# Kernel optimization log

Hardware: AMD Instinct MI355X
Metric: run time of the kernel (lower is better)

Reference implementation:

```python
import jax, jax.numpy as jnp
import numpy as np

PH, PW = 7, 7            # pooled_height, pooled_width
SCALE = 0.0625           # spatial_scale = 1/16


def setup_inputs() -> dict:
    key = jax.random.key(0)
    k1, k2, k3, k4 = jax.random.split(key, 4)
    N, C, H, W, R = 4, 512, 64, 64, 2000
    features = jax.random.normal(k1, (N, C, H, W), jnp.float32)
    # rois: (batch_idx, x1, y1, x2, y2) in image coords (image = H/SCALE x W/SCALE)
    b = jax.random.randint(k2, (R,), 0, N).astype(jnp.float32)
    xs = jnp.sort(jax.random.uniform(k3, (R, 2), jnp.float32, 0.0, W / SCALE - 1.0), axis=1)
    ys = jnp.sort(jax.random.uniform(k4, (R, 2), jnp.float32, 0.0, H / SCALE - 1.0), axis=1)
    rois = jnp.stack([b, xs[:, 0], ys[:, 0], xs[:, 1], ys[:, 1]], axis=1)
    return {"features": features, "rois": rois}


def _roi_pool(features, rois):
    # split ROI into PH x PW bins with floor/ceil boundaries, max-pool each bin.
    N, C, H, W = features.shape
    # Max spatial extent of one bin: ceil(H/PH)+1 rows; +2 is a safe static bound.
    Kh = int(np.ceil(H / PH)) + 2
    Kw = int(np.ceil(W / PW)) + 2

    def per_roi(roi):
        b = roi[0].astype(jnp.int32)
        x1 = jnp.round(roi[1] * SCALE).astype(jnp.int32)
        y1 = jnp.round(roi[2] * SCALE).astype(jnp.int32)
        x2 = jnp.round(roi[3] * SCALE).astype(jnp.int32)
        y2 = jnp.round(roi[4] * SCALE).astype(jnp.int32)
        roi_w = jnp.maximum(x2 - x1 + 1, 1).astype(jnp.float32)
        roi_h = jnp.maximum(y2 - y1 + 1, 1).astype(jnp.float32)
        bin_h = roi_h / PH
        bin_w = roi_w / PW
        ih = jnp.arange(PH, dtype=jnp.float32)
        iw = jnp.arange(PW, dtype=jnp.float32)
        hstart = jnp.clip(jnp.floor(ih * bin_h).astype(jnp.int32) + y1, 0, H)        # [PH]
        hend = jnp.clip(jnp.ceil((ih + 1.0) * bin_h).astype(jnp.int32) + y1, 0, H)   # [PH]
        wstart = jnp.clip(jnp.floor(iw * bin_w).astype(jnp.int32) + x1, 0, W)        # [PW]
        wend = jnp.clip(jnp.ceil((iw + 1.0) * bin_w).astype(jnp.int32) + x1, 0, W)   # [PW]
        # Fixed-size windows per bin, with validity masks
        hidx = hstart[:, None] + jnp.arange(Kh)[None, :]          # [PH, Kh]
        hval = hidx < hend[:, None]
        hidx = jnp.clip(hidx, 0, H - 1)
        widx = wstart[:, None] + jnp.arange(Kw)[None, :]          # [PW, Kw]
        wval = widx < wend[:, None]
        widx = jnp.clip(widx, 0, W - 1)
        fmap = features[b]                                        # [C, H, W]
        gh = fmap[:, hidx, :]                                     # [C, PH, Kh, W]
        win = gh[:, :, :, widx]                                   # [C, PH, Kh, PW, Kw]
        valid = hval[:, :, None, None] & wval[None, None, :, :]   # [PH, Kh, PW, Kw]
        mx = jnp.where(valid[None], win, -jnp.inf).max(axis=(2, 4))  # [C, PH, PW]
        empty = (hend <= hstart)[:, None] | (wend <= wstart)[None, :]  # [PH, PW]
        return jnp.where(empty[None], jnp.zeros_like(mx), mx)

    # Sequential map over ROIs keeps peak memory at ~one ROI's window buffer.
    return jax.lax.map(per_roi, rois)  # [R, C, PH, PW]


def reference(features, rois):
    return _roi_pool(features, rois)
```

## Files before the change

kernel.cpp:

```cpp
#include <hip/hip_runtime.h>
#include <math.h>
#include <float.h>

#define PH 7
#define RLEN 32

#define C7 9586981LL

__device__ __forceinline__ long long round24(long long v) {
    if (v == 0) return 0;
    int L = 64 - __clzll((unsigned long long)v);
    int sh = L - 24;
    if (sh <= 0) return v;
    long long rem  = v & ((1LL << sh) - 1);
    long long base = v >> sh;
    long long half = 1LL << (sh - 1);
    if (rem > half || (rem == half && (base & 1))) base++;
    return base << sh;
}
__device__ __forceinline__ long long bin_q26(int roi) {
    return round24((long long)roi * C7);
}
__device__ __forceinline__ int floor_k(long long b26, int k) {
    long long v = round24((long long)k * b26);
    return (int)(v >> 26);
}
__device__ __forceinline__ int ceil_k(long long b26, int k) {
    long long v = round24((long long)k * b26);
    return (int)((v + ((1LL << 26) - 1)) >> 26);
}

__global__ void roi_bounds_kernel(const float* __restrict__ rois,
                                  int* __restrict__ wsbuf, int R) {
    int r = blockIdx.x * blockDim.x + threadIdx.x;
    if (r >= R) return;
    const int H = 64, W = 64;
    const float* roi = rois + r * 5;
    int b  = (int)roi[0];
    int x1 = (int)rintf(roi[1] * 0.0625f);
    int y1 = (int)rintf(roi[2] * 0.0625f);
    int x2 = (int)rintf(roi[3] * 0.0625f);
    int y2 = (int)rintf(roi[4] * 0.0625f);

    int roi_w = max(x2 - x1 + 1, 1);
    int roi_h = max(y2 - y1 + 1, 1);
    long long bh = bin_q26(roi_h);
    long long bw = bin_q26(roi_w);

    int* o = wsbuf + r * RLEN;
    o[0] = b;
    int ws0 = 64, we6 = 0;
    #pragma unroll
    for (int i = 0; i < PH; ++i) {
        int hs = min(max(y1 + floor_k(bh, i),     0), H);
        int he = min(max(y1 + ceil_k (bh, i + 1), 0), H);
        int wst = min(max(x1 + floor_k(bw, i),     0), W);
        int wen = min(max(x1 + ceil_k (bw, i + 1), 0), W);
        o[1 + i]  = hs;
        o[8 + i]  = he;
        o[16 + i] = wst;
        o[23 + i] = wen;
        if (i == 0) ws0 = wst;
        if (i == 6) we6 = wen;
    }
    int qs = ws0 >> 2;
    int qe = (we6 + 3) >> 2;
    o[15] = qs | (max(qe, qs) << 8);
}

__device__ __forceinline__ float4 max4(float4 a, float4 b) {
    float4 r;
    r.x = fmaxf(a.x, b.x); r.y = fmaxf(a.y, b.y);
    r.z = fmaxf(a.z, b.z); r.w = fmaxf(a.w, b.w);
    return r;
}

__global__ __launch_bounds__(256) void roipool_main(
        const float* __restrict__ features,
        const int* __restrict__ wsbuf,
        float* __restrict__ out) {
    __shared__ float cm[4][8][68];

    int r    = blockIdx.x >> 4;
    int cg   = blockIdx.x & 15;
    int wv   = threadIdx.x >> 6;
    int lane = threadIdx.x & 63;
    int chsub = lane >> 3;
    int cq8   = lane & 7;
    int c0   = (cg << 5) + (wv << 3);

    const int* B = wsbuf + r * RLEN;
    int b   = B[0];
    int qpk = B[15];
    int qs  = qpk & 255;
    int qe  = qpk >> 8;
    bool dual = (qe - qs) > 8;

    const float4* f4 = (const float4*)features;
    int cbase = ((b << 9) + c0 + chsub) << 10;
    int qabs0 = qs + cq8;
    int qabs1 = qs + 8 + cq8;
    bool m0 = qabs0 < qe;
    bool m1 = qabs1 < qe;
    int qc0 = min(qabs0, 15);
    int qc1 = min(qabs1, 15);

    int ech = (lane * 9363) >> 16;
    int epw = lane - ech * 7;
    int ews = B[16 + epw];
    int ewe = B[23 + epw];
    bool eact = lane < 56;
    const float* erow = cm[wv][ech & 7];
    float vals[PH];

    const float4 NEG4 = make_float4(-FLT_MAX, -FLT_MAX, -FLT_MAX, -FLT_MAX);
    float4 last0 = NEG4, last1 = NEG4;
    int last_h = -100;

    if (!dual) {
        #pragma unroll
        for (int ph = 0; ph < PH; ++ph) {
            int hs = B[1 + ph], he = B[8 + ph];
            if (he > hs) {
                bool reuse = (hs == last_h);
                float4 a0 = reuse ? last0 : NEG4;
                int h0 = hs + (reuse ? 1 : 0);
                int nbody = he - h0 - 1;
                int idx = cbase + (h0 << 4) + qc0;
                while (nbody >= 4) {
                    float4 v0 = f4[idx];
                    float4 v1 = f4[idx + 16];
                    float4 v2 = f4[idx + 32];
                    float4 v3 = f4[idx + 48];
                    a0 = max4(a0, max4(max4(v0, v1), max4(v2, v3)));
                    idx += 64; nbody -= 4;
                }
                if (nbody >= 2) {
                    float4 v0 = f4[idx];
                    float4 v1 = f4[idx + 16];
                    a0 = max4(a0, max4(v0, v1));
                    idx += 32; nbody -= 2;
                }
                if (nbody >= 1) a0 = max4(a0, f4[idx]);
                if (he - 1 >= h0) {
                    last0 = f4[cbase + ((he - 1) << 4) + qc0];
                    a0 = max4(a0, last0);
                }
                last_h = he - 1;
                if (m0) *(float4*)&cm[wv][chsub][qabs0 << 2] = a0;
            }
            float m = -FLT_MAX;
            int w = ews;
            for (; w + 2 <= ewe; w += 2)
                m = fmaxf(fmaxf(m, erow[w]), erow[w + 1]);
            if (w < ewe) m = fmaxf(m, erow[w]);
            bool empty = (he <= hs) || (ewe <= ews);
            vals[ph] = empty ? 0.0f : m;
        }
    } else {
        #pragma unroll
        for (int ph = 0; ph < PH; ++ph) {
            int hs = B[1 + ph], he = B[8 + ph];
            if (he > hs) {
                bool reuse = (hs == last_h);
                float4 a0 = reuse ? last0 : NEG4;
                float4 a1 = reuse ? last1 : NEG4;
                int h0 = hs + (reuse ? 1 : 0);
                int nbody = he - h0 - 1;
                int idx = cbase + (h0 << 4);
                while (nbody >= 2) {
                    float4 v00 = f4[idx + qc0];
                    float4 v01 = f4[idx + qc1];
                    float4 v10 = f4[idx + 16 + qc0];
                    float4 v11 = f4[idx + 16 + qc1];
                    a0 = max4(a0, max4(v00, v10));
                    a1 = max4(a1, max4(v01, v11));
                    idx += 32; nbody -= 2;
                }
                if (nbody >= 1) {
                    a0 = max4(a0, f4[idx + qc0]);
                    a1 = max4(a1, f4[idx + qc1]);
                }
                if (he - 1 >= h0) {
                    int fin = cbase + ((he - 1) << 4);
                    last0 = f4[fin + qc0];
                    last1 = f4[fin + qc1];
                    a0 = max4(a0, last0);
                    a1 = max4(a1, last1);
                }
                last_h = he - 1;
                if (m0) *(float4*)&cm[wv][chsub][qabs0 << 2] = a0;
                if (m1) *(float4*)&cm[wv][chsub][qabs1 << 2] = a1;
            }
            float m = -FLT_MAX;
            int w = ews;
            for (; w + 2 <= ewe; w += 2)
                m = fmaxf(fmaxf(m, erow[w]), erow[w + 1]);
            if (w < ewe) m = fmaxf(m, erow[w]);
            bool empty = (he <= hs) || (ewe <= ews);
            vals[ph] = empty ? 0.0f : m;
        }
    }

    float* stage = (float*)cm[wv];
    if (eact) {
        #pragma unroll
        for (int ph = 0; ph < PH; ++ph)
            stage[ech * 49 + ph * 7 + epw] = vals[ph];
    }
    size_t obase = ((size_t)(r << 9) + c0) * 49;
    #pragma unroll
    for (int it = 0; it < 7; ++it) {
        int f = (it << 6) + lane;
        if (f < 392) out[obase + f] = stage[f];
    }
}

extern "C" void kernel_launch(void* const* d_in, const int* in_sizes, int n_in,
                              void* d_out, int out_size, void* d_ws, size_t ws_size,
                              hipStream_t stream) {
    const float* features = (const float*)d_in[0];
    const float* rois     = (const float*)d_in[1];
    float* out = (float*)d_out;
    int* wsbuf = (int*)d_ws;

    int R = in_sizes[1] / 5;

    roi_bounds_kernel<<<(R + 255) / 256, 256, 0, stream>>>(rois, wsbuf, R);
    roipool_main<<<R * 16, 256, 0, stream>>>(features, wsbuf, out);
}
```

Baseline: 201.5 us.

## Double-buffer LDS column-max rows and lag width reduction by one pooled row

The per-row LDS scratch is split into two buffers that alternate by pooled row. The width-direction max for row ph-1 is computed after the loads for row ph have been issued, so global loads can overlap with LDS reads. Lanes whose quad falls outside the ROI now skip loads entirely, so the clamped index is dropped in favour of the raw one. This doubles LDS usage per block and adds a trailing epilogue step.

Result: faster. 193.2 us (-4.1%).

```diff
diff --git a/kernel.cpp b/kernel.cpp
--- a/kernel.cpp
+++ b/kernel.cpp
@@ -79,7 +79,8 @@
         const float* __restrict__ features,
         const int* __restrict__ wsbuf,
         float* __restrict__ out) {
-    __shared__ float cm[4][8][68];
+    __shared__ float cmA[4][8][68];
+    __shared__ float cmB[4][8][68];
 
     int r    = blockIdx.x >> 4;
     int cg   = blockIdx.x & 15;
@@ -102,7 +103,6 @@
     int qabs1 = qs + 8 + cq8;
     bool m0 = qabs0 < qe;
     bool m1 = qabs1 < qe;
-    int qc0 = min(qabs0, 15);
     int qc1 = min(qabs1, 15);
 
     int ech = (lane * 9363) >> 16;
@@ -110,8 +110,10 @@
     int ews = B[16 + epw];
     int ewe = B[23 + epw];
     bool eact = lane < 56;
-    const float* erow = cm[wv][ech & 7];
+    const float* erowA = cmA[wv][ech & 7];
+    const float* erowB = cmB[wv][ech & 7];
     float vals[PH];
+    int phs = 0, phe = 0;
 
     const float4 NEG4 = make_float4(-FLT_MAX, -FLT_MAX, -FLT_MAX, -FLT_MAX);
     float4 last0 = NEG4, last1 = NEG4;
@@ -121,12 +123,13 @@
         #pragma unroll
         for (int ph = 0; ph < PH; ++ph) {
             int hs = B[1 + ph], he = B[8 + ph];
-            if (he > hs) {
+            float (*cw)[68] = (ph & 1) ? cmB[wv] : cmA[wv];
+            if (m0 && he > hs) {
                 bool reuse = (hs == last_h);
                 float4 a0 = reuse ? last0 : NEG4;
                 int h0 = hs + (reuse ? 1 : 0);
                 int nbody = he - h0 - 1;
-                int idx = cbase + (h0 << 4) + qc0;
+                int idx = cbase + (h0 << 4) + qabs0;
                 while (nbody >= 4) {
                     float4 v0 = f4[idx];
                     float4 v1 = f4[idx + 16];
@@ -143,24 +146,28 @@
                 }
                 if (nbody >= 1) a0 = max4(a0, f4[idx]);
                 if (he - 1 >= h0) {
-                    last0 = f4[cbase + ((he - 1) << 4) + qc0];
+                    last0 = f4[cbase + ((he - 1) << 4) + qabs0];
                     a0 = max4(a0, last0);
                 }
                 last_h = he - 1;
-                if (m0) *(float4*)&cm[wv][chsub][qabs0 << 2] = a0;
-            }
-            float m = -FLT_MAX;
-            int w = ews;
-            for (; w + 2 <= ewe; w += 2)
-                m = fmaxf(fmaxf(m, erow[w]), erow[w + 1]);
-            if (w < ewe) m = fmaxf(m, erow[w]);
-            bool empty = (he <= hs) || (ewe <= ews);
-            vals[ph] = empty ? 0.0f : m;
+                *(float4*)&cw[chsub][qabs0 << 2] = a0;
+            }
+            if (ph > 0) {
+                const float* er = (ph & 1) ? erowA : erowB;
+                float m = -FLT_MAX;
+                int w = ews;
+                for (; w + 2 <= ewe; w += 2)
+                    m = fmaxf(fmaxf(m, er[w]), er[w + 1]);
+                if (w < ewe) m = fmaxf(m, er[w]);
+                vals[ph - 1] = ((phe <= phs) || (ewe <= ews)) ? 0.0f : m;
+            }
+            phs = hs; phe = he;
         }
     } else {
         #pragma unroll
         for (int ph = 0; ph < PH; ++ph) {
             int hs = B[1 + ph], he = B[8 + ph];
+            float (*cw)[68] = (ph & 1) ? cmB[wv] : cmA[wv];
             if (he > hs) {
                 bool reuse = (hs == last_h);
                 float4 a0 = reuse ? last0 : NEG4;
@@ -169,40 +176,51 @@
                 int nbody = he - h0 - 1;
                 int idx = cbase + (h0 << 4);
                 while (nbody >= 2) {
-                    float4 v00 = f4[idx + qc0];
+                    float4 v00 = f4[idx + qabs0];
                     float4 v01 = f4[idx + qc1];
-                    float4 v10 = f4[idx + 16 + qc0];
+                    float4 v10 = f4[idx + 16 + qabs0];
                     float4 v11 = f4[idx + 16 + qc1];
                     a0 = max4(a0, max4(v00, v10));
                     a1 = max4(a1, max4(v01, v11));
                     idx += 32; nbody -= 2;
                 }
                 if (nbody >= 1) {
-                    a0 = max4(a0, f4[idx + qc0]);
+                    a0 = max4(a0, f4[idx + qabs0]);
                     a1 = max4(a1, f4[idx + qc1]);
                 }
                 if (he - 1 >= h0) {
                     int fin = cbase + ((he - 1) << 4);
-                    last0 = f4[fin + qc0];
+                    last0 = f4[fin + qabs0];
                     last1 = f4[fin + qc1];
                     a0 = max4(a0, last0);
                     a1 = max4(a1, last1);
                 }
                 last_h = he - 1;
-                if (m0) *(float4*)&cm[wv][chsub][qabs0 << 2] = a0;
-                if (m1) *(float4*)&cm[wv][chsub][qabs1 << 2] = a1;
-            }
-            float m = -FLT_MAX;
-            int w = ews;
-            for (; w + 2 <= ewe; w += 2)
-                m = fmaxf(fmaxf(m, erow[w]), erow[w + 1]);
-            if (w < ewe) m = fmaxf(m, erow[w]);
-            bool empty = (he <= hs) || (ewe <= ews);
-            vals[ph] = empty ? 0.0f : m;
+                *(float4*)&cw[chsub][qabs0 << 2] = a0;
+                if (m1) *(float4*)&cw[chsub][qabs1 << 2] = a1;
+            }
+            if (ph > 0) {
+                const float* er = (ph & 1) ? erowA : erowB;
+                float m = -FLT_MAX;
+                int w = ews;
+                for (; w + 2 <= ewe; w += 2)
+                    m = fmaxf(fmaxf(m, er[w]), er[w + 1]);
+                if (w < ewe) m = fmaxf(m, er[w]);
+                vals[ph - 1] = ((phe <= phs) || (ewe <= ews)) ? 0.0f : m;
+            }
+            phs = hs; phe = he;
         }
     }
-
-    float* stage = (float*)cm[wv];
+    {
+        float m = -FLT_MAX;
+        int w = ews;
+        for (; w + 2 <= ewe; w += 2)
+            m = fmaxf(fmaxf(m, erowA[w]), erowA[w + 1]);
+        if (w < ewe) m = fmaxf(m, erowA[w]);
+        vals[PH - 1] = ((phe <= phs) || (ewe <= ews)) ? 0.0f : m;
+    }
+
+    float* stage = (float*)cmA[wv];
     if (eact) {
         #pragma unroll
         for (int ph = 0; ph < PH; ++ph)
```
